# Performance work log

Measured on AMD Instinct MI355X. Metric: run time of the kernel, lower is better.

## Reference

```python
import jax, jax.numpy as jnp
import numpy as np

S, B, T, E, H, VS, VT = 40, 32, 40, 256, 512, 50000, 50000
PAD = 0


def lstm_cell(x, h, c, Wih, Whh, b):
    # PyTorch gate order: i, f, g, o
    g = x @ Wih.T + h @ Whh.T + b
    i, f, gg, o = jnp.split(g, 4, axis=-1)
    c = jax.nn.sigmoid(f) * c + jax.nn.sigmoid(i) * jnp.tanh(gg)
    h = jax.nn.sigmoid(o) * jnp.tanh(c)
    return h, c


def run_lstm(xs, Wih, Whh, b):
    # xs: [S, B, E] -> hs [S, B, H], final (h, c)
    b_ = xs.shape[1]
    init = (jnp.zeros((b_, H), xs.dtype), jnp.zeros((b_, H), xs.dtype))
    def step(carry, x):
        h, c = lstm_cell(x, carry[0], carry[1], Wih, Whh, b)
        return (h, c), h
    (hT, cT), hs = jax.lax.scan(step, init, xs)
    return hs, hT, cT


def setup_inputs() -> dict:
    key = jax.random.key(0)
    ks = jax.random.split(key, 20)
    w = lambda k, shp: (jax.random.normal(k, shp, dtype=jnp.float32) * 0.05)
    return {
        "padded_source": jax.random.randint(ks[0], (S, B), 0, VS, dtype=jnp.int32),
        "padded_target": jax.random.randint(ks[1], (T, B), 0, VT, dtype=jnp.int32),
        "enc_masks": jnp.zeros((B, S), dtype=jnp.float32),
        "src_embed": w(ks[2], (VS, E)),
        "tgt_embed": w(ks[3], (VT, E)),
        "enc_Wih_f": w(ks[4], (4 * H, E)),
        "enc_Whh_f": w(ks[5], (4 * H, H)),
        "enc_b_f": w(ks[6], (4 * H,)),
        "enc_Wih_b": w(ks[7], (4 * H, E)),
        "enc_Whh_b": w(ks[8], (4 * H, H)),
        "enc_b_b": w(ks[9], (4 * H,)),
        "dec_Wih": w(ks[10], (4 * H, E + H)),
        "dec_Whh": w(ks[11], (4 * H, H)),
        "dec_b": w(ks[12], (4 * H,)),
        "W_h": w(ks[13], (H, 2 * H)),
        "W_c": w(ks[14], (H, 2 * H)),
        "W_att": w(ks[15], (H, 2 * H)),
        "W_comb": w(ks[16], (H, 3 * H)),
        "W_vocab": w(ks[17], (VT, H)),
    }


def reference(padded_source, padded_target, enc_masks, src_embed, tgt_embed,
              enc_Wih_f, enc_Whh_f, enc_b_f, enc_Wih_b, enc_Whh_b, enc_b_b,
              dec_Wih, dec_Whh, dec_b, W_h, W_c, W_att, W_comb, W_vocab):
    # ---- encode ----
    src_e = src_embed[padded_source]                      # [S, B, E]
    hs_f, hT_f, cT_f = run_lstm(src_e, enc_Wih_f, enc_Whh_f, enc_b_f)
    hs_b, hT_b, cT_b = run_lstm(src_e[::-1], enc_Wih_b, enc_Whh_b, enc_b_b)
    hs_b = hs_b[::-1]
    enc_hidden = jnp.concatenate([hs_f, hs_b], axis=-1).transpose(1, 0, 2)  # [B, S, 2H]
    dec_h = jnp.concatenate([hT_f, hT_b], axis=-1) @ W_h.T  # [B, H]
    dec_c = jnp.concatenate([cT_f, cT_b], axis=-1) @ W_c.T
    enc_proj = enc_hidden @ W_att.T                        # [B, S, H]

    # ---- decode (scan over target timesteps) ----
    tgt_e = tgt_embed[padded_target[:-1]]                  # [T-1, B, E]
    o0 = jnp.zeros((enc_hidden.shape[0], H), enc_hidden.dtype)

    def dstep(carry, emb_t):
        h, c, o_prev = carry
        x = jnp.concatenate([emb_t, o_prev], axis=-1)
        h, c = lstm_cell(x, h, c, dec_Wih, dec_Whh, dec_b)
        scores = jnp.einsum('bsh,bh->bs', enc_proj, h)
        scores = jnp.where(enc_masks > 0, -jnp.inf, scores)
        att = jax.nn.softmax(scores, axis=-1)
        ctx = jnp.einsum('bs,bsd->bd', att, enc_hidden)
        o_t = jnp.tanh(jnp.concatenate([h, ctx], axis=-1) @ W_comb.T)
        return (h, c, o_t), o_t

    _, outs = jax.lax.scan(dstep, (dec_h, dec_c, o0), tgt_e)  # [T-1, B, H]

    # ---- scoring ----
    logp = jax.nn.log_softmax(outs @ W_vocab.T, axis=-1)      # [T-1, B, VT]
    tgt = padded_target[1:]
    tmask = (tgt != PAD).astype(logp.dtype)
    picked = jnp.take_along_axis(logp, tgt[..., None], axis=-1)[..., 0] * tmask
    return picked.sum(axis=0)                                  # [B]
```

## Files before the change

kernel.cpp:

```cpp
#include <hip/hip_runtime.h>
#include <math.h>


#define S_LEN 40
#define BATCH 32
#define EMB   256
#define HID   512
#define G4H   2048
#define NVOC  50000
#define NDEC  39
#define NCHUNK 196
#define MROWS 1248
#define MPAD  1280

__device__ __forceinline__ float sigf(float x) { return 1.f / (1.f + expf(-x)); }

__global__ __launch_bounds__(256) void k_zero(float* __restrict__ p, int n) {
  int i = blockIdx.x * 256 + threadIdx.x;
  if (i < n) p[i] = 0.f;
}

__global__ __launch_bounds__(256) void k_embed(
    const int* __restrict__ src_ids, const int* __restrict__ tgt_ids,
    const float* __restrict__ src_emb, const float* __restrict__ tgt_emb,
    float* __restrict__ src_e, float* __restrict__ tgt_e)
{
  int row = blockIdx.x, tid = threadIdx.x;
  if (row < S_LEN*BATCH) {
    int id = src_ids[row];
    src_e[(size_t)row*EMB + tid] = src_emb[(size_t)id*EMB + tid];
  } else {
    int r = row - S_LEN*BATCH;
    int id = tgt_ids[r];
    tgt_e[(size_t)r*EMB + tid] = tgt_emb[(size_t)id*EMB + tid];
  }
}

__global__ __launch_bounds__(256) void k_gemm(
    const float* __restrict__ A, const float* __restrict__ W,
    const float* __restrict__ bias, float* __restrict__ C,
    int N, int K, int ldw, int rev)
{
  __shared__ float As[16][36];
  __shared__ float Ws[16][256];
  const int tid = threadIdx.x;
  const int tx = tid & 31, ty = tid >> 5;
  const int bn = (int)blockIdx.x << 8;
  const int bmi = (int)blockIdx.y;
  const int bm = bmi << 5;
  const int arow0 = rev ? ((S_LEN - 1 - bmi) << 5) : bm;

  float acc[4][8];
#pragma unroll
  for (int i = 0; i < 4; i++)
#pragma unroll
    for (int j = 0; j < 8; j++) acc[i][j] = 0.f;

  const int ml = tid >> 3, kl = (tid & 7) << 1;
  const float* aptr = A + (size_t)(arow0 + ml)*K + kl;
  const float* wptr = W + (size_t)(bn + tid)*ldw;

  for (int k0 = 0; k0 < K; k0 += 16) {
    const float2 av  = *(const float2*)(aptr + k0);
    const float4 w0v = *(const float4*)(wptr + k0);
    const float4 w1v = *(const float4*)(wptr + k0 + 4);
    const float4 w2v = *(const float4*)(wptr + k0 + 8);
    const float4 w3v = *(const float4*)(wptr + k0 + 12);
    __syncthreads();
    As[kl][ml]   = av.x;
    As[kl+1][ml] = av.y;
    const float wt[16] = {w0v.x,w0v.y,w0v.z,w0v.w, w1v.x,w1v.y,w1v.z,w1v.w,
                          w2v.x,w2v.y,w2v.z,w2v.w, w3v.x,w3v.y,w3v.z,w3v.w};
#pragma unroll
    for (int kk = 0; kk < 16; kk++) Ws[kk][tid] = wt[kk];
    __syncthreads();
#pragma unroll
    for (int kk = 0; kk < 16; kk++) {
      const float4 a4 = *(const float4*)&As[kk][ty << 2];
      const float4 b0 = *(const float4*)&Ws[kk][tx << 2];
      const float4 b1 = *(const float4*)&Ws[kk][128 + (tx << 2)];
      const float ar[4] = {a4.x, a4.y, a4.z, a4.w};
      const float br[8] = {b0.x, b0.y, b0.z, b0.w, b1.x, b1.y, b1.z, b1.w};
#pragma unroll
      for (int i = 0; i < 4; i++)
#pragma unroll
        for (int j = 0; j < 8; j++) acc[i][j] += ar[i]*br[j];
    }
  }
  float4 bb0 = {0,0,0,0}, bb1 = {0,0,0,0};
  if (bias) {
    bb0 = *(const float4*)&bias[bn + (tx << 2)];
    bb1 = *(const float4*)&bias[bn + 128 + (tx << 2)];
  }
#pragma unroll
  for (int i = 0; i < 4; i++) {
    const int row = bm + (ty << 2) + i;
    float4 o0 = {acc[i][0]+bb0.x, acc[i][1]+bb0.y, acc[i][2]+bb0.z, acc[i][3]+bb0.w};
    float4 o1 = {acc[i][4]+bb1.x, acc[i][5]+bb1.y, acc[i][6]+bb1.z, acc[i][7]+bb1.w};
    *(float4*)&C[(size_t)row*N + bn + (tx << 2)] = o0;
    *(float4*)&C[(size_t)row*N + bn + 128 + (tx << 2)] = o1;
  }
}

__global__ __launch_bounds__(256) void k_enc_step(
    int t,
    const float* __restrict__ xproj_f, const float* __restrict__ xproj_b,
    const float* __restrict__ Whh_f, const float* __restrict__ Whh_b,
    float* __restrict__ hs_f, float* __restrict__ hs_b,
    float* __restrict__ cs_f, float* __restrict__ cs_b)
{
  __shared__ float hb[BATCH*HID];
  const int dir = (int)blockIdx.x >> 6;
  const int j0 = ((int)blockIdx.x & 63) << 3;
  const float* xproj = dir ? xproj_b : xproj_f;
  const float* Whh   = dir ? Whh_b   : Whh_f;
  float* hs = dir ? hs_b : hs_f;
  float* cs = dir ? cs_b : cs_f;
  const int tid = threadIdx.x;

  if (t > 0) {
    const float* hprev = hs + (size_t)(t-1)*BATCH*HID;
#pragma unroll
    for (int i = 0; i < 64; i++) {
      const int idx = tid + (i << 8);
      const int r = idx >> 9, k = idx & 511;
      const int p = k >> 1;
      hb[((p*32 + ((r + p) & 31)) << 1) + (k & 1)] = hprev[idx];
    }
  }
  __syncthreads();

  const int r = tid & 31, u = tid >> 5;
  const int j = j0 + u;
  const float* xrow = xproj + (size_t)(t*BATCH + r)*G4H;
  float acc[4] = { xrow[j], xrow[HID + j], xrow[2*HID + j], xrow[3*HID + j] };

  if (t > 0) {
    const float* wp[4] = { Whh + (size_t)j*HID,           Whh + (size_t)(HID + j)*HID,
                           Whh + (size_t)(2*HID + j)*HID, Whh + (size_t)(3*HID + j)*HID };
    for (int p = 0; p < 256; p += 4) {
      float hv[8];
#pragma unroll
      for (int q = 0; q < 4; q++) {
        const float2 h2 = *(const float2*)&hb[((p+q)*32 + ((r + p + q) & 31)) << 1];
        hv[2*q] = h2.x; hv[2*q+1] = h2.y;
      }
      const int kb = p << 1;
#pragma unroll
      for (int g = 0; g < 4; g++) {
        const float4 x0 = *(const float4*)(wp[g] + kb);
        const float4 x1 = *(const float4*)(wp[g] + kb + 4);
        acc[g] += hv[0]*x0.x + hv[1]*x0.y + hv[2]*x0.z + hv[3]*x0.w
                + hv[4]*x1.x + hv[5]*x1.y + hv[6]*x1.z + hv[7]*x1.w;
      }
    }
  }
  const float cprev = (t > 0) ? cs[(size_t)(t-1)*BATCH*HID + r*HID + j] : 0.f;
  const float ig = sigf(acc[0]);
  const float fg = sigf(acc[1]);
  const float gg = tanhf(acc[2]);
  const float og = sigf(acc[3]);
  const float cn = fg*cprev + ig*gg;
  const float hn = og*tanhf(cn);
  hs[(size_t)t*BATCH*HID + r*HID + j] = hn;
  cs[(size_t)t*BATCH*HID + r*HID + j] = cn;
}

__global__ __launch_bounds__(256) void k_concat(
    const float* __restrict__ hs_f, const float* __restrict__ hs_b,
    const float* __restrict__ cs_f, const float* __restrict__ cs_b,
    float* __restrict__ enc_hid, float* __restrict__ hcat, float* __restrict__ ccat)
{
  const int blk = blockIdx.x, tid = threadIdx.x;
  if (blk < BATCH*S_LEN) {
    const int b = blk / S_LEN, s = blk - b*S_LEN;
#pragma unroll
    for (int q = 0; q < 4; q++) {
      const int d = tid + (q << 8);
      const float v = (d < HID)
        ? hs_f[(size_t)s*BATCH*HID + b*HID + d]
        : hs_b[(size_t)(S_LEN-1-s)*BATCH*HID + b*HID + (d - HID)];
      enc_hid[(size_t)blk*(2*HID) + d] = v;
    }
  } else {
    const int rr = blk - BATCH*S_LEN;
    const float* Af = (rr < 32) ? hs_f : cs_f;
    const float* Ab = (rr < 32) ? hs_b : cs_b;
    float* dst = (rr < 32) ? hcat : ccat;
    const int b2 = rr & 31;
#pragma unroll
    for (int q = 0; q < 4; q++) {
      const int d = tid + (q << 8);
      const float v = (d < HID)
        ? Af[(size_t)(S_LEN-1)*BATCH*HID + b2*HID + d]
        : Ab[(size_t)(S_LEN-1)*BATCH*HID + b2*HID + (d - HID)];
      dst[(size_t)b2*(2*HID) + d] = v;
    }
  }
}

__global__ __launch_bounds__(256) void k_dec_step(
    int t,
    const float* __restrict__ dec_xp,
    const float* __restrict__ Wih, const float* __restrict__ Whh,
    float* __restrict__ dec_hs, float* __restrict__ dec_cs,
    const float* __restrict__ outs)
{
  __shared__ float xb[BATCH*1024];
  const int j0 = (int)blockIdx.x << 3;
  const int tid = threadIdx.x;
  const float* oprev = outs   + (size_t)t*BATCH*HID;
  const float* hprev = dec_hs + (size_t)t*BATCH*HID;
#pragma unroll
  for (int i = 0; i < 128; i++) {
    const int idx = tid + (i << 8);
    const int r = idx >> 10, k = idx & 1023;
    const float v = (k < HID) ? oprev[r*HID + k] : hprev[r*HID + (k - HID)];
    const int p = k >> 1;
    xb[((p*32 + ((r + p) & 31)) << 1) + (k & 1)] = v;
  }
  __syncthreads();
  const int r = tid & 31, u = tid >> 5;
  const int j = j0 + u;
  const float* xrow = dec_xp + (size_t)(t*BATCH + r)*G4H;
  float acc[4] = { xrow[j], xrow[HID + j], xrow[2*HID + j], xrow[3*HID + j] };
  {
    const float* wp[4] = { Wih + (size_t)j*768 + 256,           Wih + (size_t)(HID + j)*768 + 256,
                           Wih + (size_t)(2*HID + j)*768 + 256, Wih + (size_t)(3*HID + j)*768 + 256 };
    for (int p = 0; p < 256; p += 4) {
      float hv[8];
#pragma unroll
      for (int q = 0; q < 4; q++) {
        const float2 h2 = *(const float2*)&xb[((p+q)*32 + ((r + p + q) & 31)) << 1];
        hv[2*q] = h2.x; hv[2*q+1] = h2.y;
      }
      const int kb = p << 1;
#pragma unroll
      for (int g = 0; g < 4; g++) {
        const float4 x0 = *(const float4*)(wp[g] + kb);
        const float4 x1 = *(const float4*)(wp[g] + kb + 4);
        acc[g] += hv[0]*x0.x + hv[1]*x0.y + hv[2]*x0.z + hv[3]*x0.w
                + hv[4]*x1.x + hv[5]*x1.y + hv[6]*x1.z + hv[7]*x1.w;
      }
    }
  }
  {
    const float* wp[4] = { Whh + (size_t)j*HID,           Whh + (size_t)(HID + j)*HID,
                           Whh + (size_t)(2*HID + j)*HID, Whh + (size_t)(3*HID + j)*HID };
    for (int p = 256; p < 512; p += 4) {
      float hv[8];
#pragma unroll
      for (int q = 0; q < 4; q++) {
        const float2 h2 = *(const float2*)&xb[((p+q)*32 + ((r + p + q) & 31)) << 1];
        hv[2*q] = h2.x; hv[2*q+1] = h2.y;
      }
      const int kb = (p - 256) << 1;
#pragma unroll
      for (int g = 0; g < 4; g++) {
        const float4 x0 = *(const float4*)(wp[g] + kb);
        const float4 x1 = *(const float4*)(wp[g] + kb + 4);
        acc[g] += hv[0]*x0.x + hv[1]*x0.y + hv[2]*x0.z + hv[3]*x0.w
                + hv[4]*x1.x + hv[5]*x1.y + hv[6]*x1.z + hv[7]*x1.w;
      }
    }
  }
  const float cprev = dec_cs[(size_t)t*BATCH*HID + r*HID + j];
  const float ig = sigf(acc[0]);
  const float fg = sigf(acc[1]);
  const float gg = tanhf(acc[2]);
  const float og = sigf(acc[3]);
  const float cn = fg*cprev + ig*gg;
  const float hn = og*tanhf(cn);
  dec_hs[(size_t)(t+1)*BATCH*HID + r*HID + j] = hn;
  dec_cs[(size_t)(t+1)*BATCH*HID + r*HID + j] = cn;
}

__global__ __launch_bounds__(256) void k_attn(
    int t,
    const float* __restrict__ dec_hs, const float* __restrict__ enc_proj,
    const float* __restrict__ enc_hid, const float* __restrict__ enc_masks,
    const float* __restrict__ W_comb, float* __restrict__ outs)
{
  __shared__ float hl[HID];
  __shared__ float ctx[2*HID];
  __shared__ float sc[S_LEN];
  const int b = (int)blockIdx.x, tid = threadIdx.x;
  const float* h = dec_hs + (size_t)(t+1)*BATCH*HID + (size_t)b*HID;
  hl[tid] = h[tid];
  hl[tid + 256] = h[tid + 256];
  __syncthreads();
  const int w = tid >> 6, lane = tid & 63;
  for (int si = w; si < S_LEN; si += 4) {
    const float* ep = enc_proj + ((size_t)b*S_LEN + si)*HID;
    float partial = 0.f;
#pragma unroll
    for (int k = 0; k < 8; k++) partial += ep[lane + (k << 6)]*hl[lane + (k << 6)];
#pragma unroll
    for (int m = 32; m >= 1; m >>= 1) partial += __shfl_xor(partial, m, 64);
    if (lane == 0) sc[si] = (enc_masks[b*S_LEN + si] > 0.f) ? -INFINITY : partial;
  }
  __syncthreads();
  float mx = -INFINITY;
  for (int s2 = 0; s2 < S_LEN; s2++) mx = fmaxf(mx, sc[s2]);
  float sm = 0.f;
  for (int s2 = 0; s2 < S_LEN; s2++) sm += expf(sc[s2] - mx);
  const float inv = 1.f/sm;
  const float myatt = (tid < S_LEN) ? expf(sc[tid] - mx)*inv : 0.f;
  __syncthreads();
  if (tid < S_LEN) sc[tid] = myatt;
  __syncthreads();
#pragma unroll
  for (int q = 0; q < 4; q++) {
    const int d = tid + (q << 8);
    float s2 = 0.f;
    for (int si = 0; si < S_LEN; si++) s2 += sc[si]*enc_hid[((size_t)b*S_LEN + si)*(2*HID) + d];
    ctx[d] = s2;
  }
  __syncthreads();
#pragma unroll
  for (int q = 0; q < 2; q++) {
    const int jj = tid + (q << 8);
    const float* wr = W_comb + (size_t)jj*1536;
    float a = 0.f;
    for (int k = 0; k < HID; k += 4) {
      const float4 w4 = *(const float4*)(wr + k);
      a += w4.x*hl[k] + w4.y*hl[k+1] + w4.z*hl[k+2] + w4.w*hl[k+3];
    }
    for (int k = 0; k < 2*HID; k += 4) {
      const float4 w4 = *(const float4*)(wr + HID + k);
      a += w4.x*ctx[k] + w4.y*ctx[k+1] + w4.z*ctx[k+2] + w4.w*ctx[k+3];
    }
    outs[(size_t)(t+1)*BATCH*HID + (size_t)b*HID + jj] = tanhf(a);
  }
}

__global__ __launch_bounds__(256) void k_vocab(
    const float* __restrict__ A, const float* __restrict__ W,
    const int* __restrict__ ptgt,
    float* __restrict__ pmax, float* __restrict__ psum, float* __restrict__ picked)
{
  __shared__ float As[16][68];
  __shared__ float Ws[16][256];
  const int tid = threadIdx.x;
  const int tx = tid & 31, ty = tid >> 5;
  const int bn = (int)blockIdx.x << 8;
  const int bm = (int)blockIdx.y << 6;

  float acc[8][8];
#pragma unroll
  for (int i = 0; i < 8; i++)
#pragma unroll
    for (int j = 0; j < 8; j++) acc[i][j] = 0.f;

  const int ml = tid >> 2, kl = (tid & 3) << 2;
  const float* aptr = A + (size_t)(bm + ml)*HID + kl;
  int wrow = bn + tid; if (wrow >= NVOC) wrow = NVOC - 1;
  const float* wptr = W + (size_t)wrow*HID;

  for (int k0 = 0; k0 < HID; k0 += 16) {
    const float4 av  = *(const float4*)(aptr + k0);
    const float4 w0v = *(const float4*)(wptr + k0);
    const float4 w1v = *(const float4*)(wptr + k0 + 4);
    const float4 w2v = *(const float4*)(wptr + k0 + 8);
    const float4 w3v = *(const float4*)(wptr + k0 + 12);
    __syncthreads();
    As[kl][ml] = av.x; As[kl+1][ml] = av.y; As[kl+2][ml] = av.z; As[kl+3][ml] = av.w;
    const float wt[16] = {w0v.x,w0v.y,w0v.z,w0v.w, w1v.x,w1v.y,w1v.z,w1v.w,
                          w2v.x,w2v.y,w2v.z,w2v.w, w3v.x,w3v.y,w3v.z,w3v.w};
#pragma unroll
    for (int kk = 0; kk < 16; kk++) Ws[kk][tid] = wt[kk];
    __syncthreads();
#pragma unroll
    for (int kk = 0; kk < 16; kk++) {
      const float4 a0 = *(const float4*)&As[kk][ty << 3];
      const float4 a1 = *(const float4*)&As[kk][(ty << 3) + 4];
      const float4 b0 = *(const float4*)&Ws[kk][tx << 2];
      const float4 b1 = *(const float4*)&Ws[kk][128 + (tx << 2)];
      const float ar[8] = {a0.x,a0.y,a0.z,a0.w, a1.x,a1.y,a1.z,a1.w};
      const float br[8] = {b0.x,b0.y,b0.z,b0.w, b1.x,b1.y,b1.z,b1.w};
#pragma unroll
      for (int i = 0; i < 8; i++)
#pragma unroll
        for (int j = 0; j < 8; j++) acc[i][j] += ar[i]*br[j];
    }
  }
#pragma unroll
  for (int i = 0; i < 8; i++) {
    const int row = bm + (ty << 3) + i;
    float mx = -INFINITY;
#pragma unroll
    for (int j = 0; j < 8; j++) {
      const int col = bn + ((j < 4) ? (tx << 2) + j : 128 + (tx << 2) + j - 4);
      if (col < NVOC) mx = fmaxf(mx, acc[i][j]);
    }
#pragma unroll
    for (int m = 16; m >= 1; m >>= 1) mx = fmaxf(mx, __shfl_xor(mx, m, 32));
    float sm = 0.f;
#pragma unroll
    for (int j = 0; j < 8; j++) {
      const int col = bn + ((j < 4) ? (tx << 2) + j : 128 + (tx << 2) + j - 4);
      if (col < NVOC) sm += expf(acc[i][j] - mx);
    }
#pragma unroll
    for (int m = 16; m >= 1; m >>= 1) sm += __shfl_xor(sm, m, 32);
    if (tx == 0) {
      pmax[(size_t)row*NCHUNK + blockIdx.x] = mx;
      psum[(size_t)row*NCHUNK + blockIdx.x] = sm;
    }
    if (row < MROWS) {
      const int tt = row >> 5, bb = row & 31;
      const int tv = ptgt[(tt + 1)*BATCH + bb];
      const int rel = tv - bn;
      if (rel >= 0 && rel < 256) {
#pragma unroll
        for (int j = 0; j < 8; j++) {
          const int cl = (j < 4) ? (tx << 2) + j : 128 + (tx << 2) + j - 4;
          if (cl == rel) picked[row] = acc[i][j];
        }
      }
    }
  }
}

__global__ __launch_bounds__(256) void k_final(
    const float* __restrict__ pmax, const float* __restrict__ psum,
    const float* __restrict__ picked, const int* __restrict__ ptgt,
    float* __restrict__ out)
{
  __shared__ float red[8];
  const int b = (int)blockIdx.x, tid = threadIdx.x;
  const int lane = tid & 63, w = tid >> 6;
  float accum = 0.f;
  for (int t = 0; t < NDEC; t++) {
    const int row = t*BATCH + b;
    const float* pm = pmax + (size_t)row*NCHUNK;
    const float* ps = psum + (size_t)row*NCHUNK;
    float mx = -INFINITY;
    for (int c = tid; c < NCHUNK; c += 256) mx = fmaxf(mx, pm[c]);
#pragma unroll
    for (int m = 32; m >= 1; m >>= 1) mx = fmaxf(mx, __shfl_xor(mx, m, 64));
    if (lane == 0) red[w] = mx;
    __syncthreads();
    mx = fmaxf(fmaxf(red[0], red[1]), fmaxf(red[2], red[3]));
    __syncthreads();
    float sm = 0.f;
    for (int c = tid; c < NCHUNK; c += 256) sm += ps[c]*expf(pm[c] - mx);
#pragma unroll
    for (int m = 32; m >= 1; m >>= 1) sm += __shfl_xor(sm, m, 64);
    if (lane == 0) red[w] = sm;
    __syncthreads();
    sm = red[0] + red[1] + red[2] + red[3];
    __syncthreads();
    if (tid == 0) {
      const int tv = ptgt[(t + 1)*BATCH + b];
      if (tv != 0) accum += picked[row] - (mx + logf(sm));
    }
  }
  if (tid == 0) out[b] = accum;
}

extern "C" void kernel_launch(void* const* d_in, const int* in_sizes, int n_in,
                              void* d_out, int out_size, void* d_ws, size_t ws_size,
                              hipStream_t stream) {
  (void)in_sizes; (void)n_in; (void)out_size; (void)ws_size;
  const int*   p_src     = (const int*)d_in[0];
  const int*   p_tgt     = (const int*)d_in[1];
  const float* enc_masks = (const float*)d_in[2];
  const float* src_embed = (const float*)d_in[3];
  const float* tgt_embed = (const float*)d_in[4];
  const float* Wih_f = (const float*)d_in[5];
  const float* Whh_f = (const float*)d_in[6];
  const float* b_f   = (const float*)d_in[7];
  const float* Wih_b = (const float*)d_in[8];
  const float* Whh_b = (const float*)d_in[9];
  const float* b_b   = (const float*)d_in[10];
  const float* dWih  = (const float*)d_in[11];
  const float* dWhh  = (const float*)d_in[12];
  const float* db    = (const float*)d_in[13];
  const float* W_h   = (const float*)d_in[14];
  const float* W_c   = (const float*)d_in[15];
  const float* W_att = (const float*)d_in[16];
  const float* W_comb= (const float*)d_in[17];
  const float* W_voc = (const float*)d_in[18];
  float* out = (float*)d_out;

  float* p = (float*)d_ws;
  float* src_e    = p; p += S_LEN*BATCH*EMB;
  float* tgt_e    = p; p += NDEC*BATCH*EMB;
  float* xproj_f  = p; p += S_LEN*BATCH*G4H;
  float* xproj_b  = p; p += S_LEN*BATCH*G4H;
  float* dec_xp   = p; p += NDEC*BATCH*G4H;
  float* hs_f     = p; p += S_LEN*BATCH*HID;
  float* hs_b     = p; p += S_LEN*BATCH*HID;
  float* cs_f     = p; p += S_LEN*BATCH*HID;
  float* cs_b     = p; p += S_LEN*BATCH*HID;
  float* enc_hid  = p; p += BATCH*S_LEN*2*HID;
  float* enc_proj = p; p += BATCH*S_LEN*HID;
  float* hcat     = p; p += BATCH*2*HID;
  float* ccat     = p; p += BATCH*2*HID;
  float* dec_hs   = p; p += (NDEC+1)*BATCH*HID;
  float* dec_cs   = p; p += (NDEC+1)*BATCH*HID;
  float* outs     = p; p += (NDEC+2)*BATCH*HID;
  float* pmaxb    = p; p += (size_t)MPAD*NCHUNK;
  float* psumb    = p; p += (size_t)MPAD*NCHUNK;
  float* pickedb  = p; p += MPAD;

  k_zero<<<64, 256, 0, stream>>>(outs, BATCH*HID);
  k_zero<<<64, 256, 0, stream>>>(outs + (size_t)(NDEC+1)*BATCH*HID, BATCH*HID);

  k_embed<<<S_LEN*BATCH + NDEC*BATCH, 256, 0, stream>>>(p_src, p_tgt, src_embed, tgt_embed, src_e, tgt_e);

  k_gemm<<<dim3(8, 40), 256, 0, stream>>>(src_e, Wih_f, b_f, xproj_f, G4H, EMB, EMB, 0);
  k_gemm<<<dim3(8, 40), 256, 0, stream>>>(src_e, Wih_b, b_b, xproj_b, G4H, EMB, EMB, 1);
  k_gemm<<<dim3(8, NDEC), 256, 0, stream>>>(tgt_e, dWih, db, dec_xp, G4H, EMB, 768, 0);

  for (int t = 0; t < S_LEN; t++)
    k_enc_step<<<128, 256, 0, stream>>>(t, xproj_f, xproj_b, Whh_f, Whh_b, hs_f, hs_b, cs_f, cs_b);

  k_concat<<<BATCH*S_LEN + 64, 256, 0, stream>>>(hs_f, hs_b, cs_f, cs_b, enc_hid, hcat, ccat);

  k_gemm<<<dim3(2, 40), 256, 0, stream>>>(enc_hid, W_att, nullptr, enc_proj, HID, 2*HID, 2*HID, 0);
  k_gemm<<<dim3(2, 1), 256, 0, stream>>>(hcat, W_h, nullptr, dec_hs, HID, 2*HID, 2*HID, 0);
  k_gemm<<<dim3(2, 1), 256, 0, stream>>>(ccat, W_c, nullptr, dec_cs, HID, 2*HID, 2*HID, 0);

  for (int t = 0; t < NDEC; t++) {
    k_dec_step<<<64, 256, 0, stream>>>(t, dec_xp, dWih, dWhh, dec_hs, dec_cs, outs);
    k_attn<<<32, 256, 0, stream>>>(t, dec_hs, enc_proj, enc_hid, enc_masks, W_comb, outs);
  }

  k_vocab<<<dim3(NCHUNK, MPAD/64), 256, 0, stream>>>(outs + BATCH*HID, W_voc, p_tgt, pmaxb, psumb, pickedb);
  k_final<<<32, 256, 0, stream>>>(pmaxb, psumb, pickedb, p_tgt, out);
}
```

Measured before the change: 7.847 ms.

## Fuse encoder and decoder time loops into persistent cooperative kernels with grid sync

Replaces the per-timestep launches (40 encoder steps, plus 39×2 decoder step and attention launches) with two persistent cooperative kernels of 256 blocks that loop over time and use grid.sync between phases. Cell state stays in registers, and hidden states are stored in an interleaved layout so float4 loads can be shared across the batch. The decoder W_comb projection is now spread across all blocks instead of 32. This removes launch overhead and spreads the recurrent matvec over more CUs, at the cost of frequent grid-wide barriers and attention running on only 32 blocks while the rest wait.

```diff
diff --git a/kernel.cpp b/kernel.cpp
--- a/kernel.cpp
+++ b/kernel.cpp
@@ -1,5 +1,8 @@
 #include <hip/hip_runtime.h>
+#include <hip/hip_cooperative_groups.h>
 #include <math.h>
+
+namespace cg = cooperative_groups;
 
 
 #define S_LEN 40
@@ -15,11 +18,6 @@
 
 __device__ __forceinline__ float sigf(float x) { return 1.f / (1.f + expf(-x)); }
 
-__global__ __launch_bounds__(256) void k_zero(float* __restrict__ p, int n) {
-  int i = blockIdx.x * 256 + threadIdx.x;
-  if (i < n) p[i] = 0.f;
-}
-
 __global__ __launch_bounds__(256) void k_embed(
     const int* __restrict__ src_ids, const int* __restrict__ tgt_ids,
     const float* __restrict__ src_emb, const float* __restrict__ tgt_emb,
@@ -102,235 +100,229 @@
   }
 }
 
-__global__ __launch_bounds__(256) void k_enc_step(
-    int t,
-    const float* __restrict__ xproj_f, const float* __restrict__ xproj_b,
-    const float* __restrict__ Whh_f, const float* __restrict__ Whh_b,
-    float* __restrict__ hs_f, float* __restrict__ hs_b,
-    float* __restrict__ cs_f, float* __restrict__ cs_b)
-{
-  __shared__ float hb[BATCH*HID];
-  const int dir = (int)blockIdx.x >> 6;
-  const int j0 = ((int)blockIdx.x & 63) << 3;
-  const float* xproj = dir ? xproj_b : xproj_f;
-  const float* Whh   = dir ? Whh_b   : Whh_f;
-  float* hs = dir ? hs_b : hs_f;
-  float* cs = dir ? cs_b : cs_f;
+__global__ __launch_bounds__(256) void k_enc(
+    const float* __restrict__ xpf, const float* __restrict__ xpb,
+    const float* __restrict__ Whf, const float* __restrict__ Whb,
+    float* __restrict__ hpf, float* __restrict__ hpb,
+    float* __restrict__ hcat, float* __restrict__ ccat)
+{
+  cg::grid_group grid = cg::this_grid();
+  const int blk = blockIdx.x;
+  const int dir = blk >> 7;
+  const int ub  = blk & 127;
   const int tid = threadIdx.x;
-
-  if (t > 0) {
-    const float* hprev = hs + (size_t)(t-1)*BATCH*HID;
-#pragma unroll
-    for (int i = 0; i < 64; i++) {
-      const int idx = tid + (i << 8);
-      const int r = idx >> 9, k = idx & 511;
-      const int p = k >> 1;
-      hb[((p*32 + ((r + p) & 31)) << 1) + (k & 1)] = hprev[idx];
-    }
-  }
-  __syncthreads();
-
-  const int r = tid & 31, u = tid >> 5;
-  const int j = j0 + u;
-  const float* xrow = xproj + (size_t)(t*BATCH + r)*G4H;
-  float acc[4] = { xrow[j], xrow[HID + j], xrow[2*HID + j], xrow[3*HID + j] };
-
-  if (t > 0) {
-    const float* wp[4] = { Whh + (size_t)j*HID,           Whh + (size_t)(HID + j)*HID,
-                           Whh + (size_t)(2*HID + j)*HID, Whh + (size_t)(3*HID + j)*HID };
-    for (int p = 0; p < 256; p += 4) {
-      float hv[8];
-#pragma unroll
-      for (int q = 0; q < 4; q++) {
-        const float2 h2 = *(const float2*)&hb[((p+q)*32 + ((r + p + q) & 31)) << 1];
-        hv[2*q] = h2.x; hv[2*q+1] = h2.y;
-      }
-      const int kb = p << 1;
-#pragma unroll
-      for (int g = 0; g < 4; g++) {
-        const float4 x0 = *(const float4*)(wp[g] + kb);
-        const float4 x1 = *(const float4*)(wp[g] + kb + 4);
-        acc[g] += hv[0]*x0.x + hv[1]*x0.y + hv[2]*x0.z + hv[3]*x0.w
-                + hv[4]*x1.x + hv[5]*x1.y + hv[6]*x1.z + hv[7]*x1.w;
-      }
-    }
-  }
-  const float cprev = (t > 0) ? cs[(size_t)(t-1)*BATCH*HID + r*HID + j] : 0.f;
-  const float ig = sigf(acc[0]);
-  const float fg = sigf(acc[1]);
-  const float gg = tanhf(acc[2]);
-  const float og = sigf(acc[3]);
-  const float cn = fg*cprev + ig*gg;
-  const float hn = og*tanhf(cn);
-  hs[(size_t)t*BATCH*HID + r*HID + j] = hn;
-  cs[(size_t)t*BATCH*HID + r*HID + j] = cn;
+  const int w = tid >> 6, lane = tid & 63;
+  const int r = lane & 31, half = lane >> 5;
+  const int j = ub*4 + w;
+  const int kbase = half << 8;
+
+  const float* xp  = dir ? xpb : xpf;
+  const float* Whh = dir ? Whb : Whf;
+  float* hp = dir ? hpb : hpf;
+
+  const float* w0 = Whh + (size_t)(0*HID + j)*HID + kbase;
+  const float* w1 = Whh + (size_t)(1*HID + j)*HID + kbase;
+  const float* w2 = Whh + (size_t)(2*HID + j)*HID + kbase;
+  const float* w3 = Whh + (size_t)(3*HID + j)*HID + kbase;
+
+  float creg = 0.f;
+  for (int t = 0; t < S_LEN; t++) {
+    float a0 = 0.f, a1 = 0.f, a2 = 0.f, a3 = 0.f;
+    if (t > 0) {
+      const float* hb = hp + (size_t)(t-1)*16384 + (kbase << 5) + (r << 2);
+#pragma unroll 4
+      for (int kk = 0; kk < 256; kk += 4) {
+        const float4 hv = *(const float4*)(hb + (kk << 5));
+        const float4 v0 = *(const float4*)(w0 + kk);
+        const float4 v1 = *(const float4*)(w1 + kk);
+        const float4 v2 = *(const float4*)(w2 + kk);
+        const float4 v3 = *(const float4*)(w3 + kk);
+        a0 += v0.x*hv.x + v0.y*hv.y + v0.z*hv.z + v0.w*hv.w;
+        a1 += v1.x*hv.x + v1.y*hv.y + v1.z*hv.z + v1.w*hv.w;
+        a2 += v2.x*hv.x + v2.y*hv.y + v2.z*hv.z + v2.w*hv.w;
+        a3 += v3.x*hv.x + v3.y*hv.y + v3.z*hv.z + v3.w*hv.w;
+      }
+    }
+    a0 += __shfl_down(a0, 32);
+    a1 += __shfl_down(a1, 32);
+    a2 += __shfl_down(a2, 32);
+    a3 += __shfl_down(a3, 32);
+    if (half == 0) {
+      const float* xrow = xp + (size_t)(t*BATCH + r)*G4H;
+      const float gi = a0 + xrow[j];
+      const float gf = a1 + xrow[HID + j];
+      const float gg = a2 + xrow[2*HID + j];
+      const float go = a3 + xrow[3*HID + j];
+      const float cn = sigf(gf)*creg + sigf(gi)*tanhf(gg);
+      const float hn = sigf(go)*tanhf(cn);
+      creg = cn;
+      hp[(size_t)t*16384 + (j >> 2)*128 + (r << 2) + (j & 3)] = hn;
+      if (t == S_LEN-1) {
+        hcat[r*1024 + dir*HID + j] = hn;
+        ccat[r*1024 + dir*HID + j] = cn;
+      }
+    }
+    grid.sync();
+  }
 }
 
 __global__ __launch_bounds__(256) void k_concat(
-    const float* __restrict__ hs_f, const float* __restrict__ hs_b,
-    const float* __restrict__ cs_f, const float* __restrict__ cs_b,
-    float* __restrict__ enc_hid, float* __restrict__ hcat, float* __restrict__ ccat)
+    const float* __restrict__ hpf, const float* __restrict__ hpb,
+    float* __restrict__ ench)
 {
   const int blk = blockIdx.x, tid = threadIdx.x;
-  if (blk < BATCH*S_LEN) {
-    const int b = blk / S_LEN, s = blk - b*S_LEN;
-#pragma unroll
-    for (int q = 0; q < 4; q++) {
-      const int d = tid + (q << 8);
-      const float v = (d < HID)
-        ? hs_f[(size_t)s*BATCH*HID + b*HID + d]
-        : hs_b[(size_t)(S_LEN-1-s)*BATCH*HID + b*HID + (d - HID)];
-      enc_hid[(size_t)blk*(2*HID) + d] = v;
-    }
-  } else {
-    const int rr = blk - BATCH*S_LEN;
-    const float* Af = (rr < 32) ? hs_f : cs_f;
-    const float* Ab = (rr < 32) ? hs_b : cs_b;
-    float* dst = (rr < 32) ? hcat : ccat;
-    const int b2 = rr & 31;
-#pragma unroll
-    for (int q = 0; q < 4; q++) {
-      const int d = tid + (q << 8);
-      const float v = (d < HID)
-        ? Af[(size_t)(S_LEN-1)*BATCH*HID + b2*HID + d]
-        : Ab[(size_t)(S_LEN-1)*BATCH*HID + b2*HID + (d - HID)];
-      dst[(size_t)b2*(2*HID) + d] = v;
-    }
-  }
-}
-
-__global__ __launch_bounds__(256) void k_dec_step(
-    int t,
-    const float* __restrict__ dec_xp,
-    const float* __restrict__ Wih, const float* __restrict__ Whh,
-    float* __restrict__ dec_hs, float* __restrict__ dec_cs,
-    const float* __restrict__ outs)
-{
-  __shared__ float xb[BATCH*1024];
-  const int j0 = (int)blockIdx.x << 3;
-  const int tid = threadIdx.x;
-  const float* oprev = outs   + (size_t)t*BATCH*HID;
-  const float* hprev = dec_hs + (size_t)t*BATCH*HID;
-#pragma unroll
-  for (int i = 0; i < 128; i++) {
-    const int idx = tid + (i << 8);
-    const int r = idx >> 10, k = idx & 1023;
-    const float v = (k < HID) ? oprev[r*HID + k] : hprev[r*HID + (k - HID)];
-    const int p = k >> 1;
-    xb[((p*32 + ((r + p) & 31)) << 1) + (k & 1)] = v;
-  }
-  __syncthreads();
-  const int r = tid & 31, u = tid >> 5;
-  const int j = j0 + u;
-  const float* xrow = dec_xp + (size_t)(t*BATCH + r)*G4H;
-  float acc[4] = { xrow[j], xrow[HID + j], xrow[2*HID + j], xrow[3*HID + j] };
-  {
-    const float* wp[4] = { Wih + (size_t)j*768 + 256,           Wih + (size_t)(HID + j)*768 + 256,
-                           Wih + (size_t)(2*HID + j)*768 + 256, Wih + (size_t)(3*HID + j)*768 + 256 };
-    for (int p = 0; p < 256; p += 4) {
-      float hv[8];
-#pragma unroll
-      for (int q = 0; q < 4; q++) {
-        const float2 h2 = *(const float2*)&xb[((p+q)*32 + ((r + p + q) & 31)) << 1];
-        hv[2*q] = h2.x; hv[2*q+1] = h2.y;
-      }
-      const int kb = p << 1;
-#pragma unroll
-      for (int g = 0; g < 4; g++) {
-        const float4 x0 = *(const float4*)(wp[g] + kb);
-        const float4 x1 = *(const float4*)(wp[g] + kb + 4);
-        acc[g] += hv[0]*x0.x + hv[1]*x0.y + hv[2]*x0.z + hv[3]*x0.w
-                + hv[4]*x1.x + hv[5]*x1.y + hv[6]*x1.z + hv[7]*x1.w;
-      }
-    }
-  }
-  {
-    const float* wp[4] = { Whh + (size_t)j*HID,           Whh + (size_t)(HID + j)*HID,
-                           Whh + (size_t)(2*HID + j)*HID, Whh + (size_t)(3*HID + j)*HID };
-    for (int p = 256; p < 512; p += 4) {
-      float hv[8];
-#pragma unroll
-      for (int q = 0; q < 4; q++) {
-        const float2 h2 = *(const float2*)&xb[((p+q)*32 + ((r + p + q) & 31)) << 1];
-        hv[2*q] = h2.x; hv[2*q+1] = h2.y;
-      }
-      const int kb = (p - 256) << 1;
-#pragma unroll
-      for (int g = 0; g < 4; g++) {
-        const float4 x0 = *(const float4*)(wp[g] + kb);
-        const float4 x1 = *(const float4*)(wp[g] + kb + 4);
-        acc[g] += hv[0]*x0.x + hv[1]*x0.y + hv[2]*x0.z + hv[3]*x0.w
-                + hv[4]*x1.x + hv[5]*x1.y + hv[6]*x1.z + hv[7]*x1.w;
-      }
-    }
-  }
-  const float cprev = dec_cs[(size_t)t*BATCH*HID + r*HID + j];
-  const float ig = sigf(acc[0]);
-  const float fg = sigf(acc[1]);
-  const float gg = tanhf(acc[2]);
-  const float og = sigf(acc[3]);
-  const float cn = fg*cprev + ig*gg;
-  const float hn = og*tanhf(cn);
-  dec_hs[(size_t)(t+1)*BATCH*HID + r*HID + j] = hn;
-  dec_cs[(size_t)(t+1)*BATCH*HID + r*HID + j] = cn;
-}
-
-__global__ __launch_bounds__(256) void k_attn(
-    int t,
-    const float* __restrict__ dec_hs, const float* __restrict__ enc_proj,
-    const float* __restrict__ enc_hid, const float* __restrict__ enc_masks,
-    const float* __restrict__ W_comb, float* __restrict__ outs)
-{
-  __shared__ float hl[HID];
-  __shared__ float ctx[2*HID];
-  __shared__ float sc[S_LEN];
-  const int b = (int)blockIdx.x, tid = threadIdx.x;
-  const float* h = dec_hs + (size_t)(t+1)*BATCH*HID + (size_t)b*HID;
-  hl[tid] = h[tid];
-  hl[tid + 256] = h[tid + 256];
-  __syncthreads();
-  const int w = tid >> 6, lane = tid & 63;
-  for (int si = w; si < S_LEN; si += 4) {
-    const float* ep = enc_proj + ((size_t)b*S_LEN + si)*HID;
-    float partial = 0.f;
-#pragma unroll
-    for (int k = 0; k < 8; k++) partial += ep[lane + (k << 6)]*hl[lane + (k << 6)];
-#pragma unroll
-    for (int m = 32; m >= 1; m >>= 1) partial += __shfl_xor(partial, m, 64);
-    if (lane == 0) sc[si] = (enc_masks[b*S_LEN + si] > 0.f) ? -INFINITY : partial;
-  }
-  __syncthreads();
-  float mx = -INFINITY;
-  for (int s2 = 0; s2 < S_LEN; s2++) mx = fmaxf(mx, sc[s2]);
-  float sm = 0.f;
-  for (int s2 = 0; s2 < S_LEN; s2++) sm += expf(sc[s2] - mx);
-  const float inv = 1.f/sm;
-  const float myatt = (tid < S_LEN) ? expf(sc[tid] - mx)*inv : 0.f;
-  __syncthreads();
-  if (tid < S_LEN) sc[tid] = myatt;
-  __syncthreads();
+  const int b = blk / S_LEN, s = blk - b*S_LEN;
 #pragma unroll
   for (int q = 0; q < 4; q++) {
     const int d = tid + (q << 8);
-    float s2 = 0.f;
-    for (int si = 0; si < S_LEN; si++) s2 += sc[si]*enc_hid[((size_t)b*S_LEN + si)*(2*HID) + d];
-    ctx[d] = s2;
-  }
-  __syncthreads();
-#pragma unroll
-  for (int q = 0; q < 2; q++) {
-    const int jj = tid + (q << 8);
-    const float* wr = W_comb + (size_t)jj*1536;
-    float a = 0.f;
-    for (int k = 0; k < HID; k += 4) {
-      const float4 w4 = *(const float4*)(wr + k);
-      a += w4.x*hl[k] + w4.y*hl[k+1] + w4.z*hl[k+2] + w4.w*hl[k+3];
-    }
-    for (int k = 0; k < 2*HID; k += 4) {
-      const float4 w4 = *(const float4*)(wr + HID + k);
-      a += w4.x*ctx[k] + w4.y*ctx[k+1] + w4.z*ctx[k+2] + w4.w*ctx[k+3];
-    }
-    outs[(size_t)(t+1)*BATCH*HID + (size_t)b*HID + jj] = tanhf(a);
+    float v;
+    if (d < HID) v = hpf[(size_t)s*16384 + (d >> 2)*128 + (b << 2) + (d & 3)];
+    else {
+      const int d2 = d - HID;
+      v = hpb[(size_t)(S_LEN-1-s)*16384 + (d2 >> 2)*128 + (b << 2) + (d2 & 3)];
+    }
+    ench[(size_t)blk*1024 + d] = v;
+  }
+}
+
+__global__ __launch_bounds__(256) void k_dec(
+    const float* __restrict__ xproj, const float* __restrict__ Wih, const float* __restrict__ Whh,
+    const float* __restrict__ Wcomb, const float* __restrict__ encp, const float* __restrict__ ench,
+    const float* __restrict__ masks, const float* __restrict__ h0, const float* __restrict__ c0,
+    float* __restrict__ aop, float* __restrict__ xcomb, float* __restrict__ outs)
+{
+  cg::grid_group grid = cg::this_grid();
+  __shared__ float redA[4][2][4][32];
+  __shared__ float redC[4][2][32];
+  __shared__ float hl[HID];
+  __shared__ float sc[S_LEN];
+
+  const int blk = blockIdx.x, tid = threadIdx.x;
+  const int w = tid >> 6, lane = tid & 63;
+  const int r = lane & 31, half = lane >> 5;
+  const int j0 = blk*2;
+
+  const int kbA = w*256 + half*128;
+  const float* wA[8];
+#pragma unroll
+  for (int u = 0; u < 2; u++)
+#pragma unroll
+    for (int g = 0; g < 4; g++) {
+      const int row = g*HID + j0 + u;
+      wA[u*4+g] = (kbA < HID) ? (Wih + (size_t)row*768 + 256 + kbA)
+                              : (Whh + (size_t)row*HID + (kbA - HID));
+    }
+  const float* habase = aop + (kbA << 5) + (r << 2);
+
+  const int kbC = w*384 + half*192;
+  const float* wC0 = Wcomb + (size_t)(j0  )*1536 + kbC;
+  const float* wC1 = Wcomb + (size_t)(j0+1)*1536 + kbC;
+  const float* hcbase = xcomb + (kbC << 5) + (r << 2);
+
+  float creg = 0.f;
+  if (tid < 64) {
+    const int uh = tid >> 5, rr = tid & 31;
+    const int j = j0 + uh;
+    creg = c0[rr*HID + j];
+    aop[(128 + (j >> 2))*128 + (rr << 2) + (j & 3)] = h0[rr*HID + j];
+    aop[((j >> 2))*128 + (rr << 2) + (j & 3)] = 0.f;
+  }
+  grid.sync();
+
+  for (int t = 0; t < NDEC; t++) {
+    {
+      float acc8[8];
+#pragma unroll
+      for (int p = 0; p < 8; p++) acc8[p] = 0.f;
+#pragma unroll 2
+      for (int kk = 0; kk < 128; kk += 4) {
+        const float4 hv = *(const float4*)(habase + (kk << 5));
+#pragma unroll
+        for (int p = 0; p < 8; p++) {
+          const float4 wv = *(const float4*)(wA[p] + kk);
+          acc8[p] += wv.x*hv.x + wv.y*hv.y + wv.z*hv.z + wv.w*hv.w;
+        }
+      }
+#pragma unroll
+      for (int p = 0; p < 8; p++) acc8[p] += __shfl_down(acc8[p], 32);
+      if (half == 0) {
+#pragma unroll
+        for (int p = 0; p < 8; p++) redA[w][p >> 2][p & 3][r] = acc8[p];
+      }
+    }
+    __syncthreads();
+    if (tid < 64) {
+      const int uh = tid >> 5, rr = tid & 31, j = j0 + uh;
+      const float* xrow = xproj + (size_t)(t*BATCH + rr)*G4H;
+      float g4[4];
+#pragma unroll
+      for (int g = 0; g < 4; g++)
+        g4[g] = xrow[g*HID + j] + redA[0][uh][g][rr] + redA[1][uh][g][rr]
+                                + redA[2][uh][g][rr] + redA[3][uh][g][rr];
+      const float cn = sigf(g4[1])*creg + sigf(g4[0])*tanhf(g4[2]);
+      const float hn = sigf(g4[3])*tanhf(cn);
+      creg = cn;
+      xcomb[(j >> 2)*128 + (rr << 2) + (j & 3)] = hn;
+      aop[(128 + (j >> 2))*128 + (rr << 2) + (j & 3)] = hn;
+    }
+    grid.sync();
+
+    if (blk < BATCH) {
+      const int b = blk;
+      if (tid < 128) ((float4*)hl)[tid] = *(const float4*)&xcomb[tid*128 + (b << 2)];
+      __syncthreads();
+      for (int s = w; s < S_LEN; s += 4) {
+        const float* ep = encp + ((size_t)b*S_LEN + s)*HID;
+        float part = 0.f;
+#pragma unroll
+        for (int k = 0; k < 8; k++) part += ep[lane + (k << 6)]*hl[lane + (k << 6)];
+#pragma unroll
+        for (int m = 32; m >= 1; m >>= 1) part += __shfl_xor(part, m, 64);
+        if (lane == 0) sc[s] = (masks[b*S_LEN + s] > 0.f) ? -INFINITY : part;
+      }
+      __syncthreads();
+      float mx = -INFINITY;
+      for (int s2 = 0; s2 < S_LEN; s2++) mx = fmaxf(mx, sc[s2]);
+      float sm = 0.f;
+      for (int s2 = 0; s2 < S_LEN; s2++) sm += expf(sc[s2] - mx);
+      const float inv = 1.f/sm;
+      const float myatt = (tid < S_LEN) ? expf(sc[tid] - mx)*inv : 0.f;
+      __syncthreads();
+      if (tid < S_LEN) sc[tid] = myatt;
+      __syncthreads();
+#pragma unroll
+      for (int q = 0; q < 4; q++) {
+        const int d = tid + (q << 8);
+        float cd = 0.f;
+        for (int s = 0; s < S_LEN; s++) cd += sc[s]*ench[((size_t)b*S_LEN + s)*1024 + d];
+        const int k = HID + d;
+        xcomb[(k >> 2)*128 + (b << 2) + (k & 3)] = cd;
+      }
+    }
+    grid.sync();
+
+    {
+      float ca = 0.f, cb = 0.f;
+#pragma unroll 2
+      for (int kk = 0; kk < 192; kk += 4) {
+        const float4 hv = *(const float4*)(hcbase + (kk << 5));
+        const float4 v0 = *(const float4*)(wC0 + kk);
+        const float4 v1 = *(const float4*)(wC1 + kk);
+        ca += v0.x*hv.x + v0.y*hv.y + v0.z*hv.z + v0.w*hv.w;
+        cb += v1.x*hv.x + v1.y*hv.y + v1.z*hv.z + v1.w*hv.w;
+      }
+      ca += __shfl_down(ca, 32);
+      cb += __shfl_down(cb, 32);
+      if (half == 0) { redC[w][0][r] = ca; redC[w][1][r] = cb; }
+    }
+    __syncthreads();
+    if (tid < 64) {
+      const int uh = tid >> 5, rr = tid & 31, j = j0 + uh;
+      const float o = tanhf(redC[0][uh][rr] + redC[1][uh][rr] + redC[2][uh][rr] + redC[3][uh][rr]);
+      aop[(j >> 2)*128 + (rr << 2) + (j & 3)] = o;
+      outs[(size_t)(t*BATCH + rr)*HID + j] = o;
+    }
+    grid.sync();
   }
 }
 
@@ -487,47 +479,49 @@
   float* p = (float*)d_ws;
   float* src_e    = p; p += S_LEN*BATCH*EMB;
   float* tgt_e    = p; p += NDEC*BATCH*EMB;
-  float* xproj_f  = p; p += S_LEN*BATCH*G4H;
-  float* xproj_b  = p; p += S_LEN*BATCH*G4H;
+  float* xpf      = p; p += S_LEN*BATCH*G4H;
+  float* xpb      = p; p += S_LEN*BATCH*G4H;
   float* dec_xp   = p; p += NDEC*BATCH*G4H;
-  float* hs_f     = p; p += S_LEN*BATCH*HID;
-  float* hs_b     = p; p += S_LEN*BATCH*HID;
-  float* cs_f     = p; p += S_LEN*BATCH*HID;
-  float* cs_b     = p; p += S_LEN*BATCH*HID;
-  float* enc_hid  = p; p += BATCH*S_LEN*2*HID;
-  float* enc_proj = p; p += BATCH*S_LEN*HID;
+  float* hpf      = p; p += S_LEN*BATCH*HID;
+  float* hpb      = p; p += S_LEN*BATCH*HID;
   float* hcat     = p; p += BATCH*2*HID;
   float* ccat     = p; p += BATCH*2*HID;
-  float* dec_hs   = p; p += (NDEC+1)*BATCH*HID;
-  float* dec_cs   = p; p += (NDEC+1)*BATCH*HID;
-  float* outs     = p; p += (NDEC+2)*BATCH*HID;
+  float* ench     = p; p += BATCH*S_LEN*2*HID;
+  float* encp     = p; p += BATCH*S_LEN*HID;
+  float* h0       = p; p += BATCH*HID;
+  float* c0       = p; p += BATCH*HID;
+  float* aop      = p; p += 1024*BATCH;
+  float* xcomb    = p; p += 1536*BATCH;
+  float* outs     = p; p += (size_t)MPAD*HID;
   float* pmaxb    = p; p += (size_t)MPAD*NCHUNK;
   float* psumb    = p; p += (size_t)MPAD*NCHUNK;
   float* pickedb  = p; p += MPAD;
 
-  k_zero<<<64, 256, 0, stream>>>(outs, BATCH*HID);
-  k_zero<<<64, 256, 0, stream>>>(outs + (size_t)(NDEC+1)*BATCH*HID, BATCH*HID);
-
   k_embed<<<S_LEN*BATCH + NDEC*BATCH, 256, 0, stream>>>(p_src, p_tgt, src_embed, tgt_embed, src_e, tgt_e);
 
-  k_gemm<<<dim3(8, 40), 256, 0, stream>>>(src_e, Wih_f, b_f, xproj_f, G4H, EMB, EMB, 0);
-  k_gemm<<<dim3(8, 40), 256, 0, stream>>>(src_e, Wih_b, b_b, xproj_b, G4H, EMB, EMB, 1);
+  k_gemm<<<dim3(8, 40), 256, 0, stream>>>(src_e, Wih_f, b_f, xpf, G4H, EMB, EMB, 0);
+  k_gemm<<<dim3(8, 40), 256, 0, stream>>>(src_e, Wih_b, b_b, xpb, G4H, EMB, EMB, 1);
   k_gemm<<<dim3(8, NDEC), 256, 0, stream>>>(tgt_e, dWih, db, dec_xp, G4H, EMB, 768, 0);
 
-  for (int t = 0; t < S_LEN; t++)
-    k_enc_step<<<128, 256, 0, stream>>>(t, xproj_f, xproj_b, Whh_f, Whh_b, hs_f, hs_b, cs_f, cs_b);
-
-  k_concat<<<BATCH*S_LEN + 64, 256, 0, stream>>>(hs_f, hs_b, cs_f, cs_b, enc_hid, hcat, ccat);
-
-  k_gemm<<<dim3(2, 40), 256, 0, stream>>>(enc_hid, W_att, nullptr, enc_proj, HID, 2*HID, 2*HID, 0);
-  k_gemm<<<dim3(2, 1), 256, 0, stream>>>(hcat, W_h, nullptr, dec_hs, HID, 2*HID, 2*HID, 0);
-  k_gemm<<<dim3(2, 1), 256, 0, stream>>>(ccat, W_c, nullptr, dec_cs, HID, 2*HID, 2*HID, 0);
-
-  for (int t = 0; t < NDEC; t++) {
-    k_dec_step<<<64, 256, 0, stream>>>(t, dec_xp, dWih, dWhh, dec_hs, dec_cs, outs);
-    k_attn<<<32, 256, 0, stream>>>(t, dec_hs, enc_proj, enc_hid, enc_masks, W_comb, outs);
-  }
-
-  k_vocab<<<dim3(NCHUNK, MPAD/64), 256, 0, stream>>>(outs + BATCH*HID, W_voc, p_tgt, pmaxb, psumb, pickedb);
+  {
+    void* args[] = { (void*)&xpf, (void*)&xpb, (void*)&Whh_f, (void*)&Whh_b,
+                     (void*)&hpf, (void*)&hpb, (void*)&hcat, (void*)&ccat };
+    hipLaunchCooperativeKernel((void*)k_enc, dim3(256), dim3(256), args, 0, stream);
+  }
+
+  k_concat<<<BATCH*S_LEN, 256, 0, stream>>>(hpf, hpb, ench);
+
+  k_gemm<<<dim3(2, 40), 256, 0, stream>>>(ench, W_att, nullptr, encp, HID, 2*HID, 2*HID, 0);
+  k_gemm<<<dim3(2, 1), 256, 0, stream>>>(hcat, W_h, nullptr, h0, HID, 2*HID, 2*HID, 0);
+  k_gemm<<<dim3(2, 1), 256, 0, stream>>>(ccat, W_c, nullptr, c0, HID, 2*HID, 2*HID, 0);
+
+  {
+    void* args[] = { (void*)&dec_xp, (void*)&dWih, (void*)&dWhh, (void*)&W_comb,
+                     (void*)&encp, (void*)&ench, (void*)&enc_masks, (void*)&h0, (void*)&c0,
+                     (void*)&aop, (void*)&xcomb, (void*)&outs };
+    hipLaunchCooperativeKernel((void*)k_dec, dim3(256), dim3(256), args, 0, stream);
+  }
+
+  k_vocab<<<dim3(NCHUNK, MPAD/64), 256, 0, stream>>>(outs, W_voc, p_tgt, pmaxb, psumb, pickedb);
   k_final<<<32, 256, 0, stream>>>(pmaxb, psumb, pickedb, p_tgt, out);
 }
```

After: 9.120 ms. 16.2% more time.
